# Kernel tuning notes

Hardware: AMD Instinct MI355X
Metric: run time of the kernel (lower is better)

The kernel has to match this reference:

```python
import jax, jax.numpy as jnp
import numpy as np

M, K, N = 4096, 4096, 4096          # tokens, in_features, out_features
ROW_BLOCK, COL_BLOCK = 1, 4          # sparse block shape (rows x cols of W)
BLOCK_DENSITY = 0.2                  # fraction of nonzero blocks


def setup_inputs() -> dict:
    key = jax.random.key(0)
    k1, k2, k3, k4 = jax.random.split(key, 4)
    # quint8 activations stored as int32 in [0, 255]
    x_q = jax.random.randint(k1, (M, K), 0, 256, dtype=jnp.int32)
    # qint8 weights stored as int32 in [-127, 127], zero_point == 0
    w_dense = jax.random.randint(k2, (N, K), -127, 128, dtype=jnp.int32)
    # block-sparse structure: zero out whole ROW_BLOCK x COL_BLOCK blocks
    blk_mask = jax.random.bernoulli(k3, BLOCK_DENSITY, (N // ROW_BLOCK, K // COL_BLOCK))
    mask = jnp.repeat(jnp.repeat(blk_mask, ROW_BLOCK, axis=0), COL_BLOCK, axis=1)
    w_q = jnp.where(mask, w_dense, 0)
    bias = jax.random.normal(k4, (N,), dtype=jnp.float32) * 0.1
    return dict(
        x_q=x_q,
        w_q=w_q,
        bias=bias,
        x_scale=jnp.float32(0.05),
        x_zp=jnp.int32(128),
        w_scale=jnp.float32(0.01),
        out_scale=jnp.float32(0.1),
        out_zp=jnp.int32(128),
    )


def reference(x_q, w_q, bias, x_scale, x_zp, w_scale, out_scale, out_zp):
    # int32 accumulate of (x - x_zp) @ W^T over the (block-)sparse weight
    acc = jnp.einsum('mk,nk->mn', x_q - x_zp, w_q)  # [M, N] int32
    # dequantize + bias
    y = acc.astype(jnp.float32) * (x_scale * w_scale) + bias[None, :]
    # requantize to quint8 (stored as int32)
    q = jnp.round(y / out_scale).astype(jnp.int32) + out_zp
    return jnp.clip(q, 0, 255)
```

## Files before the change

### kernel.cpp

```cpp
#include <hip/hip_runtime.h>
#include <stdint.h>

#define MDIM 4096
#define NDIM 4096
#define KDIM 4096
#define BM 256
#define BN 256
#define BKB 128
#define NT (KDIM / BKB)

typedef int i32x4 __attribute__((ext_vector_type(4)));

typedef __attribute__((address_space(1))) const void gv_t;
typedef __attribute__((address_space(3))) void lv_t;

#define BAR() do { asm volatile("" ::: "memory"); __builtin_amdgcn_s_barrier(); asm volatile("" ::: "memory"); } while (0)
#define LGKM0_BAR() do { asm volatile("s_waitcnt lgkmcnt(0)" ::: "memory"); BAR(); } while (0)

__device__ __forceinline__ int pack4(int a, int b, int c, int d) {
    return (a & 0xFF) | ((b & 0xFF) << 8) | ((c & 0xFF) << 16) | ((d & 0xFF) << 24);
}

__global__ void pack_x_kernel(const int* __restrict__ x, const int* __restrict__ zp_p,
                              int* __restrict__ out, int total4) {
    const int zp = zp_p[0];
    int i = blockIdx.x * blockDim.x + threadIdx.x;
    if (i < total4) {
        int4 a = ((const int4*)x)[i];
        out[i] = pack4(a.x - zp, a.y - zp, a.z - zp, a.w - zp);
    }
}

__global__ void pack_w_kernel(const int* __restrict__ w, int* __restrict__ out, int total4) {
    int i = blockIdx.x * blockDim.x + threadIdx.x;
    if (i < total4) {
        int4 a = ((const int4*)w)[i];
        out[i] = pack4(a.x, a.y, a.z, a.w);
    }
}

__global__ __launch_bounds__(512, 2)
void gemm_i8_8ph(const char* __restrict__ A8, const char* __restrict__ B8,
                 const float* __restrict__ bias,
                 const float* __restrict__ xs_p, const float* __restrict__ ws_p,
                 const float* __restrict__ os_p, const int* __restrict__ ozp_p,
                 int* __restrict__ out) {
    __shared__ char lds[131072];

    const int t = threadIdx.x;
    const int lane = t & 63;
    const int wave = t >> 6;
    const int wr = wave >> 2;
    const int wc = wave & 3;

    int wg = blockIdx.x;
    int swz = (wg & 7) * (256 / 8) + (wg >> 3);
    const long brow = (long)(swz >> 4) * BM;
    const long bcol = (long)(swz & 15) * BN;

    i32x4 acc[8][4] = {};

    int aoff[8][2], boff[4][2];
    #pragma unroll
    for (int mi = 0; mi < 8; ++mi) {
        int row = wr * 128 + mi * 16 + (lane & 15);
        #pragma unroll
        for (int kk = 0; kk < 2; ++kk) {
            int ls = kk * 4 + (lane >> 4);
            aoff[mi][kk] = row * BKB + ((ls ^ (row & 7)) * 16);
        }
    }
    #pragma unroll
    for (int ni = 0; ni < 4; ++ni) {
        int row = wc * 64 + ni * 16 + (lane & 15);
        #pragma unroll
        for (int kk = 0; kk < 2; ++kk) {
            int ls = kk * 4 + (lane >> 4);
            boff[ni][kk] = 65536 + row * BKB + ((ls ^ (row & 7)) * 16);
        }
    }
    const char* sbase[4][2];
    int ldsoff[4][2];
    #pragma unroll
    for (int h = 0; h < 4; ++h) {
        const char* src = (h < 2) ? A8 : B8;
        long rc = (h < 2) ? brow : bcol;
        #pragma unroll
        for (int j = 0; j < 2; ++j) {
            int chunk = (h & 1) * 1024 + t + j * 512;
            int row = chunk >> 3, slot = chunk & 7;
            sbase[h][j] = src + (rc + row) * KDIM + ((slot ^ (row & 7)) * 16);
            ldsoff[h][j] = ((h < 2) ? 0 : 65536) + chunk * 16;
        }
    }

#define STAGE(tt_, h_) do { \
    if ((tt_) < NT) { \
        int dd_ = ((tt_) & 1) * 32768; \
        __builtin_amdgcn_global_load_lds((gv_t*)(sbase[h_][0] + (long)(tt_) * BKB), \
                                         (lv_t*)(lds + dd_ + ldsoff[h_][0]), 16, 0, 0); \
        __builtin_amdgcn_global_load_lds((gv_t*)(sbase[h_][1] + (long)(tt_) * BKB), \
                                         (lv_t*)(lds + dd_ + ldsoff[h_][1]), 16, 0, 0); \
    } } while (0)

#define MFMA_Q(MLO, NLO) do { \
    __builtin_amdgcn_s_setprio(1); \
    _Pragma("unroll") \
    for (int mi = MLO; mi < MLO + 4; ++mi) \
        _Pragma("unroll") \
        for (int ni = NLO; ni < NLO + 2; ++ni) \
            _Pragma("unroll") \
            for (int kk = 0; kk < 2; ++kk) \
                acc[mi][ni] = __builtin_amdgcn_mfma_i32_16x16x64_i8(af[mi][kk], bf[ni][kk], acc[mi][ni], 0, 0, 0); \
    __builtin_amdgcn_s_setprio(0); \
} while (0)

    STAGE(0, 0); STAGE(0, 1); STAGE(0, 2); STAGE(0, 3);
    STAGE(1, 0); STAGE(1, 1);
    asm volatile("s_waitcnt vmcnt(4)" ::: "memory");
    BAR();

    i32x4 af[8][2], bf[4][2];

    #pragma unroll 2
    for (int tt = 0; tt < NT; ++tt) {
        const int dpar = (tt & 1) * 32768;

        #pragma unroll
        for (int mi = 0; mi < 4; ++mi)
            #pragma unroll
            for (int kk = 0; kk < 2; ++kk)
                af[mi][kk] = *(const i32x4*)(lds + dpar + aoff[mi][kk]);
        #pragma unroll
        for (int ni = 0; ni < 2; ++ni)
            #pragma unroll
            for (int kk = 0; kk < 2; ++kk)
                bf[ni][kk] = *(const i32x4*)(lds + dpar + boff[ni][kk]);
        STAGE(tt + 1, 2);
        BAR();
        MFMA_Q(0, 0);
        LGKM0_BAR();

        #pragma unroll
        for (int mi = 4; mi < 8; ++mi)
            #pragma unroll
            for (int kk = 0; kk < 2; ++kk)
                af[mi][kk] = *(const i32x4*)(lds + dpar + aoff[mi][kk]);
        STAGE(tt + 1, 3);
        BAR();
        MFMA_Q(4, 0);
        LGKM0_BAR();

        #pragma unroll
        for (int ni = 2; ni < 4; ++ni)
            #pragma unroll
            for (int kk = 0; kk < 2; ++kk)
                bf[ni][kk] = *(const i32x4*)(lds + dpar + boff[ni][kk]);
        STAGE(tt + 2, 0);
        BAR();
        MFMA_Q(0, 2);
        LGKM0_BAR();

        STAGE(tt + 2, 1);
        BAR();
        MFMA_Q(4, 2);
        if (tt >= NT - 2)      asm volatile("s_waitcnt vmcnt(0)" ::: "memory");
        else                   asm volatile("s_waitcnt vmcnt(4)" ::: "memory");
        BAR();
    }
#undef STAGE
#undef MFMA_Q

    const float scale = xs_p[0] * ws_p[0];
    const float os = os_p[0];
    const int ozp = ozp_p[0];
    #pragma unroll
    for (int mi = 0; mi < 8; ++mi) {
        long row0 = brow + wr * 128 + mi * 16 + (lane >> 4) * 4;
        #pragma unroll
        for (int ni = 0; ni < 4; ++ni) {
            long col = bcol + wc * 64 + ni * 16 + (lane & 15);
            float bv = bias[col];
            #pragma unroll
            for (int r = 0; r < 4; ++r) {
                float y = (float)acc[mi][ni][r] * scale + bv;
                int q = (int)rintf(y / os) + ozp;
                q = q < 0 ? 0 : (q > 255 ? 255 : q);
                out[(row0 + r) * NDIM + col] = q;
            }
        }
    }
}

__global__ void naive_gemm_kernel(const int* __restrict__ x, const int* __restrict__ w,
                                  const float* __restrict__ bias,
                                  const float* __restrict__ xs_p, const int* __restrict__ xzp_p,
                                  const float* __restrict__ ws_p, const float* __restrict__ os_p,
                                  const int* __restrict__ ozp_p, int* __restrict__ out) {
    long idx = (long)blockIdx.x * blockDim.x + threadIdx.x;
    if (idx >= (long)MDIM * NDIM) return;
    int m = idx >> 12, n = idx & (NDIM - 1);
    const int4* xr = (const int4*)(x + (long)m * KDIM);
    const int4* wv = (const int4*)(w + (long)n * KDIM);
    const int zp = xzp_p[0];
    int acc = 0;
    for (int k = 0; k < KDIM / 4; ++k) {
        int4 a = xr[k], b = wv[k];
        acc += (a.x - zp) * b.x + (a.y - zp) * b.y + (a.z - zp) * b.z + (a.w - zp) * b.w;
    }
    float y = (float)acc * (xs_p[0] * ws_p[0]) + bias[n];
    int q = (int)rintf(y / os_p[0]) + ozp_p[0];
    out[idx] = q < 0 ? 0 : (q > 255 ? 255 : q);
}

extern "C" void kernel_launch(void* const* d_in, const int* in_sizes, int n_in,
                              void* d_out, int out_size, void* d_ws, size_t ws_size,
                              hipStream_t stream) {
    const int*   x_q  = (const int*)d_in[0];
    const int*   w_q  = (const int*)d_in[1];
    const float* bias = (const float*)d_in[2];
    const float* xs   = (const float*)d_in[3];
    const int*   xzp  = (const int*)d_in[4];
    const float* wsc  = (const float*)d_in[5];
    const float* osc  = (const float*)d_in[6];
    const int*   ozp  = (const int*)d_in[7];
    int* out = (int*)d_out;

    const size_t need = 2UL * MDIM * KDIM;
    if (ws_size >= need) {
        char* A8 = (char*)d_ws;
        char* B8 = A8 + (size_t)MDIM * KDIM;
        const int total4 = MDIM * KDIM / 4;
        pack_x_kernel<<<total4 / 256, 256, 0, stream>>>(x_q, xzp, (int*)A8, total4);
        pack_w_kernel<<<total4 / 256, 256, 0, stream>>>(w_q, (int*)B8, total4);
        gemm_i8_8ph<<<(MDIM / BM) * (NDIM / BN), 512, 0, stream>>>(
            A8, B8, bias, xs, wsc, osc, ozp, out);
    } else {
        long total = (long)MDIM * NDIM;
        naive_gemm_kernel<<<(total + 255) / 256, 256, 0, stream>>>(
            x_q, w_q, bias, xs, xzp, wsc, osc, ozp, out);
    }
}
```

Measured before the change: 263.8 us.

## Replace 8-phase interleaved pipeline with single-barrier double-buffered main loop

Restructures the int8 GEMM main loop so each K-tile issues all global-to-LDS loads for the next tile up front, reads every A/B fragment from LDS, runs all 64 MFMAs, then waits and hits one barrier. This drops the 8 barriers per iteration and the staggered partial-stage prefetch. The trade-off is a full vmcnt(0) wait every iteration and less fine-grained overlap of loads with MFMA work. It also holds more fragment registers live at once.

```diff
diff --git a/kernel.cpp b/kernel.cpp
--- a/kernel.cpp
+++ b/kernel.cpp
@@ -15,7 +15,6 @@
 typedef __attribute__((address_space(3))) void lv_t;
 
 #define BAR() do { asm volatile("" ::: "memory"); __builtin_amdgcn_s_barrier(); asm volatile("" ::: "memory"); } while (0)
-#define LGKM0_BAR() do { asm volatile("s_waitcnt lgkmcnt(0)" ::: "memory"); BAR(); } while (0)
 
 __device__ __forceinline__ int pack4(int a, int b, int c, int d) {
     return (a & 0xFF) | ((b & 0xFF) << 8) | ((c & 0xFF) << 16) | ((d & 0xFF) << 24);
@@ -40,11 +39,11 @@
 }
 
 __global__ __launch_bounds__(512, 2)
-void gemm_i8_8ph(const char* __restrict__ A8, const char* __restrict__ B8,
-                 const float* __restrict__ bias,
-                 const float* __restrict__ xs_p, const float* __restrict__ ws_p,
-                 const float* __restrict__ os_p, const int* __restrict__ ozp_p,
-                 int* __restrict__ out) {
+void gemm_i8_1bar(const char* __restrict__ A8, const char* __restrict__ B8,
+                  const float* __restrict__ bias,
+                  const float* __restrict__ xs_p, const float* __restrict__ ws_p,
+                  const float* __restrict__ os_p, const int* __restrict__ ozp_p,
+                  int* __restrict__ out) {
     __shared__ char lds[131072];
 
     const int t = threadIdx.x;
@@ -94,30 +93,19 @@
         }
     }
 
-#define STAGE(tt_, h_) do { \
+#define STAGE_ALL(tt_, dd_) do { \
     if ((tt_) < NT) { \
-        int dd_ = ((tt_) & 1) * 32768; \
-        __builtin_amdgcn_global_load_lds((gv_t*)(sbase[h_][0] + (long)(tt_) * BKB), \
-                                         (lv_t*)(lds + dd_ + ldsoff[h_][0]), 16, 0, 0); \
-        __builtin_amdgcn_global_load_lds((gv_t*)(sbase[h_][1] + (long)(tt_) * BKB), \
-                                         (lv_t*)(lds + dd_ + ldsoff[h_][1]), 16, 0, 0); \
+        _Pragma("unroll") \
+        for (int h = 0; h < 4; ++h) { \
+            __builtin_amdgcn_global_load_lds((gv_t*)(sbase[h][0] + (long)(tt_) * BKB), \
+                                             (lv_t*)(lds + (dd_) + ldsoff[h][0]), 16, 0, 0); \
+            __builtin_amdgcn_global_load_lds((gv_t*)(sbase[h][1] + (long)(tt_) * BKB), \
+                                             (lv_t*)(lds + (dd_) + ldsoff[h][1]), 16, 0, 0); \
+        } \
     } } while (0)
 
-#define MFMA_Q(MLO, NLO) do { \
-    __builtin_amdgcn_s_setprio(1); \
-    _Pragma("unroll") \
-    for (int mi = MLO; mi < MLO + 4; ++mi) \
-        _Pragma("unroll") \
-        for (int ni = NLO; ni < NLO + 2; ++ni) \
-            _Pragma("unroll") \
-            for (int kk = 0; kk < 2; ++kk) \
-                acc[mi][ni] = __builtin_amdgcn_mfma_i32_16x16x64_i8(af[mi][kk], bf[ni][kk], acc[mi][ni], 0, 0, 0); \
-    __builtin_amdgcn_s_setprio(0); \
-} while (0)
-
-    STAGE(0, 0); STAGE(0, 1); STAGE(0, 2); STAGE(0, 3);
-    STAGE(1, 0); STAGE(1, 1);
-    asm volatile("s_waitcnt vmcnt(4)" ::: "memory");
+    STAGE_ALL(0, 0);
+    asm volatile("s_waitcnt vmcnt(0)" ::: "memory");
     BAR();
 
     i32x4 af[8][2], bf[4][2];
@@ -125,6 +113,9 @@
     #pragma unroll 2
     for (int tt = 0; tt < NT; ++tt) {
         const int dpar = (tt & 1) * 32768;
+        const int dnxt = dpar ^ 32768;
+
+        STAGE_ALL(tt + 1, dnxt);
 
         #pragma unroll
         for (int mi = 0; mi < 4; ++mi)
@@ -136,40 +127,52 @@
             #pragma unroll
             for (int kk = 0; kk < 2; ++kk)
                 bf[ni][kk] = *(const i32x4*)(lds + dpar + boff[ni][kk]);
-        STAGE(tt + 1, 2);
+        #pragma unroll
+        for (int mi = 4; mi < 8; ++mi)
+            #pragma unroll
+            for (int kk = 0; kk < 2; ++kk)
+                af[mi][kk] = *(const i32x4*)(lds + dpar + aoff[mi][kk]);
+        #pragma unroll
+        for (int ni = 2; ni < 4; ++ni)
+            #pragma unroll
+            for (int kk = 0; kk < 2; ++kk)
+                bf[ni][kk] = *(const i32x4*)(lds + dpar + boff[ni][kk]);
+
+        __builtin_amdgcn_s_setprio(1);
+        #pragma unroll
+        for (int mi = 0; mi < 4; ++mi)
+            #pragma unroll
+            for (int ni = 0; ni < 2; ++ni)
+                #pragma unroll
+                for (int kk = 0; kk < 2; ++kk)
+                    acc[mi][ni] = __builtin_amdgcn_mfma_i32_16x16x64_i8(af[mi][kk], bf[ni][kk], acc[mi][ni], 0, 0, 0);
+        #pragma unroll
+        for (int mi = 4; mi < 8; ++mi)
+            #pragma unroll
+            for (int ni = 0; ni < 2; ++ni)
+                #pragma unroll
+                for (int kk = 0; kk < 2; ++kk)
+                    acc[mi][ni] = __builtin_amdgcn_mfma_i32_16x16x64_i8(af[mi][kk], bf[ni][kk], acc[mi][ni], 0, 0, 0);
+        #pragma unroll
+        for (int mi = 0; mi < 4; ++mi)
+            #pragma unroll
+            for (int ni = 2; ni < 4; ++ni)
+                #pragma unroll
+                for (int kk = 0; kk < 2; ++kk)
+                    acc[mi][ni] = __builtin_amdgcn_mfma_i32_16x16x64_i8(af[mi][kk], bf[ni][kk], acc[mi][ni], 0, 0, 0);
+        #pragma unroll
+        for (int mi = 4; mi < 8; ++mi)
+            #pragma unroll
+            for (int ni = 2; ni < 4; ++ni)
+                #pragma unroll
+                for (int kk = 0; kk < 2; ++kk)
+                    acc[mi][ni] = __builtin_amdgcn_mfma_i32_16x16x64_i8(af[mi][kk], bf[ni][kk], acc[mi][ni], 0, 0, 0);
+        __builtin_amdgcn_s_setprio(0);
+
+        asm volatile("s_waitcnt vmcnt(0) lgkmcnt(0)" ::: "memory");
         BAR();
-        MFMA_Q(0, 0);
-        LGKM0_BAR();
-
-        #pragma unroll
-        for (int mi = 4; mi < 8; ++mi)
-            #pragma unroll
-            for (int kk = 0; kk < 2; ++kk)
-                af[mi][kk] = *(const i32x4*)(lds + dpar + aoff[mi][kk]);
-        STAGE(tt + 1, 3);
-        BAR();
-        MFMA_Q(4, 0);
-        LGKM0_BAR();
-
-        #pragma unroll
-        for (int ni = 2; ni < 4; ++ni)
-            #pragma unroll
-            for (int kk = 0; kk < 2; ++kk)
-                bf[ni][kk] = *(const i32x4*)(lds + dpar + boff[ni][kk]);
-        STAGE(tt + 2, 0);
-        BAR();
-        MFMA_Q(0, 2);
-        LGKM0_BAR();
-
-        STAGE(tt + 2, 1);
-        BAR();
-        MFMA_Q(4, 2);
-        if (tt >= NT - 2)      asm volatile("s_waitcnt vmcnt(0)" ::: "memory");
-        else                   asm volatile("s_waitcnt vmcnt(4)" ::: "memory");
-        BAR();
-    }
-#undef STAGE
-#undef MFMA_Q
+    }
+#undef STAGE_ALL
 
     const float scale = xs_p[0] * ws_p[0];
     const float os = os_p[0];
@@ -233,7 +236,7 @@
         const int total4 = MDIM * KDIM / 4;
         pack_x_kernel<<<total4 / 256, 256, 0, stream>>>(x_q, xzp, (int*)A8, total4);
         pack_w_kernel<<<total4 / 256, 256, 0, stream>>>(w_q, (int*)B8, total4);
-        gemm_i8_8ph<<<(MDIM / BM) * (NDIM / BN), 512, 0, stream>>>(
+        gemm_i8_1bar<<<(MDIM / BM) * (NDIM / BN), 512, 0, stream>>>(
             A8, B8, bias, xs, wsc, osc, ozp, out);
     } else {
         long total = (long)MDIM * NDIM;
```

Result: slower. 274.7 us (+4.1%).

## Switch int8 GEMM to 32x32x32 MFMA and restructure LDS pipeline

Applied to the files above, without the earlier changes.

Replaces the 16x16x64 int8 MFMA tiling with 32x32x32 MFMA instructions, so each wave holds 4x2 accumulators of 16 registers each, and rewrites the LDS fragment offsets and epilogue mapping to match. All A/B fragments for a K-tile are now loaded up front, and the prefetch schedule is rearranged so three of the four staging halves are issued one step ahead, with a different vmcnt wait. The larger MFMA shape cuts instruction count and raises operand reuse per LDS read. In exchange it needs more fragment registers held live, and the extra barriers per phase may add synchronisation stalls.

```diff
diff --git a/kernel.cpp b/kernel.cpp
--- a/kernel.cpp
+++ b/kernel.cpp
@@ -9,13 +9,13 @@
 #define BKB 128
 #define NT (KDIM / BKB)
 
-typedef int i32x4 __attribute__((ext_vector_type(4)));
+typedef int i32x4  __attribute__((ext_vector_type(4)));
+typedef int i32x16 __attribute__((ext_vector_type(16)));
 
 typedef __attribute__((address_space(1))) const void gv_t;
 typedef __attribute__((address_space(3))) void lv_t;
 
 #define BAR() do { asm volatile("" ::: "memory"); __builtin_amdgcn_s_barrier(); asm volatile("" ::: "memory"); } while (0)
-#define LGKM0_BAR() do { asm volatile("s_waitcnt lgkmcnt(0)" ::: "memory"); BAR(); } while (0)
 
 __device__ __forceinline__ int pack4(int a, int b, int c, int d) {
     return (a & 0xFF) | ((b & 0xFF) << 8) | ((c & 0xFF) << 16) | ((d & 0xFF) << 24);
@@ -40,11 +40,11 @@
 }
 
 __global__ __launch_bounds__(512, 2)
-void gemm_i8_8ph(const char* __restrict__ A8, const char* __restrict__ B8,
-                 const float* __restrict__ bias,
-                 const float* __restrict__ xs_p, const float* __restrict__ ws_p,
-                 const float* __restrict__ os_p, const int* __restrict__ ozp_p,
-                 int* __restrict__ out) {
+void gemm_i8_32x32(const char* __restrict__ A8, const char* __restrict__ B8,
+                   const float* __restrict__ bias,
+                   const float* __restrict__ xs_p, const float* __restrict__ ws_p,
+                   const float* __restrict__ os_p, const int* __restrict__ ozp_p,
+                   int* __restrict__ out) {
     __shared__ char lds[131072];
 
     const int t = threadIdx.x;
@@ -58,25 +58,25 @@
     const long brow = (long)(swz >> 4) * BM;
     const long bcol = (long)(swz & 15) * BN;
 
-    i32x4 acc[8][4] = {};
-
-    int aoff[8][2], boff[4][2];
-    #pragma unroll
-    for (int mi = 0; mi < 8; ++mi) {
-        int row = wr * 128 + mi * 16 + (lane & 15);
-        #pragma unroll
-        for (int kk = 0; kk < 2; ++kk) {
-            int ls = kk * 4 + (lane >> 4);
-            aoff[mi][kk] = row * BKB + ((ls ^ (row & 7)) * 16);
-        }
-    }
-    #pragma unroll
-    for (int ni = 0; ni < 4; ++ni) {
-        int row = wc * 64 + ni * 16 + (lane & 15);
-        #pragma unroll
-        for (int kk = 0; kk < 2; ++kk) {
-            int ls = kk * 4 + (lane >> 4);
-            boff[ni][kk] = 65536 + row * BKB + ((ls ^ (row & 7)) * 16);
+    i32x16 acc[4][2] = {};
+
+    int aoff[4][4], boff[2][4];
+    #pragma unroll
+    for (int mi = 0; mi < 4; ++mi) {
+        int row = wr * 128 + mi * 32 + (lane & 31);
+        #pragma unroll
+        for (int j = 0; j < 4; ++j) {
+            int ls = j * 2 + (lane >> 5);
+            aoff[mi][j] = row * BKB + ((ls ^ (row & 7)) * 16);
+        }
+    }
+    #pragma unroll
+    for (int ni = 0; ni < 2; ++ni) {
+        int row = wc * 64 + ni * 32 + (lane & 31);
+        #pragma unroll
+        for (int j = 0; j < 4; ++j) {
+            int ls = j * 2 + (lane >> 5);
+            boff[ni][j] = 65536 + row * BKB + ((ls ^ (row & 7)) * 16);
         }
     }
     const char* sbase[4][2];
@@ -103,69 +103,60 @@
                                          (lv_t*)(lds + dd_ + ldsoff[h_][1]), 16, 0, 0); \
     } } while (0)
 
-#define MFMA_Q(MLO, NLO) do { \
+#define MFMA_Q(MLO, NI) do { \
     __builtin_amdgcn_s_setprio(1); \
     _Pragma("unroll") \
-    for (int mi = MLO; mi < MLO + 4; ++mi) \
+    for (int mi = MLO; mi < MLO + 2; ++mi) \
         _Pragma("unroll") \
-        for (int ni = NLO; ni < NLO + 2; ++ni) \
-            _Pragma("unroll") \
-            for (int kk = 0; kk < 2; ++kk) \
-                acc[mi][ni] = __builtin_amdgcn_mfma_i32_16x16x64_i8(af[mi][kk], bf[ni][kk], acc[mi][ni], 0, 0, 0); \
+        for (int j = 0; j < 4; ++j) \
+            acc[mi][NI] = __builtin_amdgcn_mfma_i32_32x32x32_i8(af[mi][j], bf[NI][j], acc[mi][NI], 0, 0, 0); \
     __builtin_amdgcn_s_setprio(0); \
 } while (0)
 
     STAGE(0, 0); STAGE(0, 1); STAGE(0, 2); STAGE(0, 3);
-    STAGE(1, 0); STAGE(1, 1);
+    STAGE(1, 0); STAGE(1, 1); STAGE(1, 2);
     asm volatile("s_waitcnt vmcnt(4)" ::: "memory");
     BAR();
 
-    i32x4 af[8][2], bf[4][2];
+    i32x4 af[4][4], bf[2][4];
 
     #pragma unroll 2
     for (int tt = 0; tt < NT; ++tt) {
         const int dpar = (tt & 1) * 32768;
 
+        STAGE(tt + 1, 3);
+        if (tt == NT - 1) asm volatile("s_waitcnt vmcnt(0)" ::: "memory");
+        else              asm volatile("s_waitcnt vmcnt(8)" ::: "memory");
+        BAR();
+
         #pragma unroll
         for (int mi = 0; mi < 4; ++mi)
             #pragma unroll
-            for (int kk = 0; kk < 2; ++kk)
-                af[mi][kk] = *(const i32x4*)(lds + dpar + aoff[mi][kk]);
+            for (int j = 0; j < 4; ++j)
+                af[mi][j] = *(const i32x4*)(lds + dpar + aoff[mi][j]);
         #pragma unroll
         for (int ni = 0; ni < 2; ++ni)
             #pragma unroll
-            for (int kk = 0; kk < 2; ++kk)
-                bf[ni][kk] = *(const i32x4*)(lds + dpar + boff[ni][kk]);
-        STAGE(tt + 1, 2);
-        BAR();
+            for (int j = 0; j < 4; ++j)
+                bf[ni][j] = *(const i32x4*)(lds + dpar + boff[ni][j]);
+
         MFMA_Q(0, 0);
-        LGKM0_BAR();
-
-        #pragma unroll
-        for (int mi = 4; mi < 8; ++mi)
-            #pragma unroll
-            for (int kk = 0; kk < 2; ++kk)
-                af[mi][kk] = *(const i32x4*)(lds + dpar + aoff[mi][kk]);
-        STAGE(tt + 1, 3);
-        BAR();
-        MFMA_Q(4, 0);
-        LGKM0_BAR();
-
-        #pragma unroll
-        for (int ni = 2; ni < 4; ++ni)
-            #pragma unroll
-            for (int kk = 0; kk < 2; ++kk)
-                bf[ni][kk] = *(const i32x4*)(lds + dpar + boff[ni][kk]);
+        asm volatile("s_waitcnt lgkmcnt(0)" ::: "memory");
+        BAR();
+
         STAGE(tt + 2, 0);
         BAR();
-        MFMA_Q(0, 2);
-        LGKM0_BAR();
+        MFMA_Q(0, 1);
+        BAR();
 
         STAGE(tt + 2, 1);
         BAR();
-        MFMA_Q(4, 2);
-        if (tt >= NT - 2)      asm volatile("s_waitcnt vmcnt(0)" ::: "memory");
-        else                   asm volatile("s_waitcnt vmcnt(4)" ::: "memory");
+        MFMA_Q(2, 0);
+        BAR();
+
+        STAGE(tt + 2, 2);
+        BAR();
+        MFMA_Q(2, 1);
         BAR();
     }
 #undef STAGE
@@ -175,18 +166,19 @@
     const float os = os_p[0];
     const int ozp = ozp_p[0];
     #pragma unroll
-    for (int mi = 0; mi < 8; ++mi) {
-        long row0 = brow + wr * 128 + mi * 16 + (lane >> 4) * 4;
-        #pragma unroll
-        for (int ni = 0; ni < 4; ++ni) {
-            long col = bcol + wc * 64 + ni * 16 + (lane & 15);
+    for (int mi = 0; mi < 4; ++mi) {
+        long rowb = brow + wr * 128 + mi * 32 + 4 * (lane >> 5);
+        #pragma unroll
+        for (int ni = 0; ni < 2; ++ni) {
+            long col = bcol + wc * 64 + ni * 32 + (lane & 31);
             float bv = bias[col];
             #pragma unroll
-            for (int r = 0; r < 4; ++r) {
-                float y = (float)acc[mi][ni][r] * scale + bv;
+            for (int reg = 0; reg < 16; ++reg) {
+                long row = rowb + (reg & 3) + 8 * (reg >> 2);
+                float y = (float)acc[mi][ni][reg] * scale + bv;
                 int q = (int)rintf(y / os) + ozp;
                 q = q < 0 ? 0 : (q > 255 ? 255 : q);
-                out[(row0 + r) * NDIM + col] = q;
+                out[row * NDIM + col] = q;
             }
         }
     }
@@ -233,7 +225,7 @@
         const int total4 = MDIM * KDIM / 4;
         pack_x_kernel<<<total4 / 256, 256, 0, stream>>>(x_q, xzp, (int*)A8, total4);
         pack_w_kernel<<<total4 / 256, 256, 0, stream>>>(w_q, (int*)B8, total4);
-        gemm_i8_8ph<<<(MDIM / BM) * (NDIM / BN), 512, 0, stream>>>(
+        gemm_i8_32x32<<<(MDIM / BM) * (NDIM / BN), 512, 0, stream>>>(
             A8, B8, bias, xs, wsc, osc, ozp, out);
     } else {
         long total = (long)MDIM * NDIM;
```

After: 306.9 us. 1.16x slower.
